# Performance work log

Hardware: AMD Instinct MI355X
Metric: run time of the kernel (lower is better)

## Reference

```python
import jax, jax.numpy as jnp
import numpy as np

B, L, D, H, WIN, EXP = 2, 4096, 1024, 16, 256, 4

def setup_inputs() -> dict:
    key = jax.random.key(0)
    ks = jax.random.split(key, 8)
    F = EXP * D
    p = lambda k, shape: jax.random.normal(k, shape, dtype=jnp.float32) * 0.02
    return {
        "x": jax.random.normal(ks[0], (B, L, D), dtype=jnp.float32),
        "mask": jnp.zeros((B, L), dtype=jnp.float32),  # 0 = local attention everywhere
        "Wq": p(ks[1], (D, D)), "bq": jnp.zeros((D,), jnp.float32),
        "Wk": p(ks[2], (D, D)), "bk": jnp.zeros((D,), jnp.float32),
        "Wv": p(ks[3], (D, D)), "bv": jnp.zeros((D,), jnp.float32),
        "ln_g": jnp.ones((D,), jnp.float32), "ln_b": jnp.zeros((D,), jnp.float32),
        "W1": p(ks[4], (D, F)), "b1": jnp.zeros((F,), jnp.float32),
        "W2": p(ks[5], (F, D)), "b2": jnp.zeros((D,), jnp.float32),
    }


def reference(x, mask, Wq, bq, Wk, bk, Wv, bv, ln_g, ln_b, W1, b1, W2, b2):
    NEG = jnp.asarray(-1e9, x.dtype)
    Bs, Ls, Ds = x.shape
    dh = Ds // H
    c = WIN // 2  # one-sided window size (HF uses attention_window // 2)
    pad = WIN - Ls % WIN
    xp = jnp.pad(x, ((0, 0), (0, pad), (0, 0)))  # pad_token_id == 0
    mp = jnp.pad(mask, ((0, 0), (0, pad)), constant_values=-10000.0)
    S = Ls + pad
    n = S // c  # number of query chunks of size c

    inv_sqrt_dh = jnp.asarray(1.0 / np.sqrt(dh), x.dtype)
    q = ((xp @ Wq + bq) * inv_sqrt_dh).reshape(Bs, S, H, dh)
    k = (xp @ Wk + bk).reshape(Bs, S, H, dh)
    v = (xp @ Wv + bv).reshape(Bs, S, H, dh)

    # pad keys/values by one chunk on each side so query chunk i sees chunks i-1,i,i+1
    kp = jnp.pad(k, ((0, 0), (c, c), (0, 0), (0, 0)))
    vp = jnp.pad(v, ((0, 0), (c, c), (0, 0), (0, 0)))
    kvalid = jnp.pad(mp == 0.0, ((0, 0), (c, c)), constant_values=False)  # [B, S+2c]

    idx = jnp.arange(n)[:, None] * c + jnp.arange(3 * c)[None, :]  # [n, 3c]
    kc = kp[:, idx]   # [B, n, 3c, H, dh]
    vc = vp[:, idx]   # [B, n, 3c, H, dh]
    kvc = kvalid[:, idx]  # [B, n, 3c]
    qc = q.reshape(Bs, n, c, H, dh)

    scores = jnp.einsum('bnphd,bnrhd->bhnpr', qc, kc)  # [B,H,n,c,3c]
    p_ = jnp.arange(c)[:, None]
    r_ = jnp.arange(3 * c)[None, :]
    band = (r_ >= p_) & (r_ <= p_ + 2 * c)  # exact |i-j| <= c band, [c,3c]
    valid = band[None, None, None, :, :] & kvc[:, None, :, None, :]
    scores = jnp.where(valid, scores, NEG)
    probs = jax.nn.softmax(scores, axis=-1)
    attn = jnp.einsum('bhnpr,bnrhd->bnphd', probs, vc).reshape(Bs, S, Ds)

    h = (xp + attn)[:, :Ls]  # residual then drop padding (matches module order)
    mu = jnp.mean(h, axis=-1, keepdims=True)
    var = jnp.var(h, axis=-1, keepdims=True)
    h = (h - mu) / jnp.sqrt(var + 1e-5) * ln_g + ln_b
    out = h + (jax.nn.gelu(h @ W1 + b1, approximate=False) @ W2 + b2)
    return out
```

## Files before the change

kernel.cpp:

```cpp
#include <hip/hip_runtime.h>
#include <hip/hip_bf16.h>
#include <cstdint>

typedef __attribute__((ext_vector_type(8))) short short8;
typedef __attribute__((ext_vector_type(4))) short short4v;
typedef __attribute__((ext_vector_type(4))) float floatx4;

constexpr int B_ = 2, L_ = 4096, D_ = 1024, H_ = 16, DH = 64, F_ = 4096;
constexpr int M_ = B_ * L_;
constexpr int NQKV = 3 * D_;
constexpr int VT_GUARD = 512;

constexpr size_t OFF_XB  = 0;
constexpr size_t OFF_WCT = OFF_XB  + (size_t)M_ * D_ * 2;
constexpr size_t OFF_W1T = OFF_WCT + (size_t)NQKV * D_ * 2;
constexpr size_t OFF_W2T = OFF_W1T + (size_t)F_ * D_ * 2;
constexpr size_t OFF_QKV = OFF_W2T + (size_t)D_ * F_ * 2;
constexpr size_t OFF_VT  = OFF_QKV + (size_t)M_ * NQKV * 2;
constexpr size_t OFF_ATT = OFF_VT  + ((size_t)B_*H_*DH*L_ + 2*VT_GUARD) * 2;
constexpr size_t OFF_HB  = OFF_ATT + (size_t)M_ * D_ * 2;
constexpr size_t OFF_MID = OFF_HB  + (size_t)M_ * D_ * 2;

static __device__ __forceinline__ float b2f(unsigned short u) {
    union { unsigned int i; float f; } v; v.i = ((unsigned int)u) << 16; return v.f;
}

static __device__ __forceinline__ void gload16(const void* g, void* l) {
    __builtin_amdgcn_global_load_lds(
        (const __attribute__((address_space(1))) uint32_t*)g,
        (__attribute__((address_space(3))) uint32_t*)l, 16, 0, 0);
}

__global__ __launch_bounds__(256) void k_cvt_x(const float* __restrict__ x,
                                               __hip_bfloat16* __restrict__ xb) {
    int i = (blockIdx.x * 256 + threadIdx.x) * 8;
    float4 a = *(const float4*)(x + i);
    float4 b = *(const float4*)(x + i + 4);
    alignas(16) __hip_bfloat16 t[8];
    t[0] = __float2bfloat16(a.x); t[1] = __float2bfloat16(a.y);
    t[2] = __float2bfloat16(a.z); t[3] = __float2bfloat16(a.w);
    t[4] = __float2bfloat16(b.x); t[5] = __float2bfloat16(b.y);
    t[6] = __float2bfloat16(b.z); t[7] = __float2bfloat16(b.w);
    *(uint4*)(xb + i) = *(const uint4*)t;
}

__global__ __launch_bounds__(256) void k_tcvt(const float* __restrict__ in,
                                              __hip_bfloat16* __restrict__ out,
                                              int R, int C) {
    __shared__ float t[64][65];
    int tx = threadIdx.x & 63, ty4 = threadIdx.x >> 6;
    int c0 = blockIdx.x * 64, r0 = blockIdx.y * 64;
#pragma unroll
    for (int i = 0; i < 16; i++) {
        int r = ty4 + i * 4;
        t[r][tx] = in[(size_t)(r0 + r) * C + c0 + tx];
    }
    __syncthreads();
#pragma unroll
    for (int i = 0; i < 16; i++) {
        int r = ty4 + i * 4;
        out[(size_t)(c0 + r) * R + r0 + tx] = __float2bfloat16(t[tx][r]);
    }
}

__global__ __launch_bounds__(256) void k_vtrans(const __hip_bfloat16* __restrict__ qkv,
                                                __hip_bfloat16* __restrict__ vtg) {
    __shared__ __hip_bfloat16 t[64][72];
    int tx = threadIdx.x & 63, ty4 = threadIdx.x >> 6;
    int bh = blockIdx.y, b = bh >> 4, h = bh & 15;
    int j0 = blockIdx.x * 64;
#pragma unroll
    for (int i = 0; i < 16; i++) {
        int j = ty4 + i * 4;
        t[j][tx] = qkv[(size_t)(b * L_ + j0 + j) * NQKV + 2 * D_ + h * DH + tx];
    }
    __syncthreads();
#pragma unroll
    for (int i = 0; i < 16; i++) {
        int d = ty4 + i * 4;
        vtg[(long)(bh * DH + d) * L_ + j0 + tx] = t[tx][d];
    }
}

template<int NFRAG, int GM, int EPI, int KTOT, int NBN>
__global__ __launch_bounds__(512, 2)
void k_g8(const __hip_bfloat16* __restrict__ A, const __hip_bfloat16* __restrict__ BT,
          const float* __restrict__ b0p, const float* __restrict__ b1p,
          const float* __restrict__ b2p,
          __hip_bfloat16* __restrict__ obf, float* __restrict__ of32,
          const __hip_bfloat16* __restrict__ hres) {
    constexpr int BN = NFRAG * 64;
    constexpr int KT = KTOT / 64;
    constexpr int PER = GM * NBN;

    __shared__ __hip_bfloat16 AS[2][4 * 4096];
    __shared__ __hip_bfloat16 BS[2][NFRAG * 4096];

    const int tid = threadIdx.x, wave = tid >> 6, lane = tid & 63;
    const int lo = lane & 15, hi = lane >> 4;
    const int wm = wave >> 2, wn = wave & 3;

    const int nwg = gridDim.x, q = nwg >> 3;
    const int bid = blockIdx.x;
    const int swz = (bid & 7) * q + (bid >> 3);
    const int g = swz / PER, r = swz % PER;
    const int bm = g * GM + (r % GM);
    const int bn = r / GM;
    const size_t m0 = (size_t)bm * 256, n0 = (size_t)bn * BN;

    const int srow = tid >> 3;
    const int gcc = (tid & 7) ^ (srow & 7);
    const __hip_bfloat16* aG = A  + (m0 + srow) * (size_t)KTOT + gcc * 8;
    const __hip_bfloat16* bG = BT + (n0 + srow) * (size_t)KTOT + gcc * 8;
    const int ldst = wave * 512;

    int ccr[2];
#pragma unroll
    for (int k = 0; k < 2; ++k) ccr[k] = ((k * 4 + hi) ^ (lo & 7)) * 8;
    const int Ra = wm * 128 + lo;
    const int Rb0 = wn * (NFRAG * 16) + lo;

    floatx4 acc[8][NFRAG] = {};

#define STG_A(buf, sw, tn) gload16(aG + (size_t)(sw) * 64 * KTOT + (size_t)(tn) * 64, \
                                   &AS[buf][(sw) * 4096 + ldst])
#define STG_B(buf, sw, tn) gload16(bG + (size_t)(sw) * 64 * KTOT + (size_t)(tn) * 64, \
                                   &BS[buf][(sw) * 4096 + ldst])

    STG_B(0, 0, 0); STG_B(0, 1, 0);
    if (NFRAG == 4) { STG_B(0, 2, 0); STG_B(0, 3, 0); }
    STG_A(0, 0, 0); STG_A(0, 2, 0); STG_A(0, 1, 0); STG_A(0, 3, 0);
    asm volatile("s_waitcnt vmcnt(0)" ::: "memory");
    __builtin_amdgcn_s_barrier();

    for (int t = 0; t < KT; ++t) {
        const int cur = t & 1, nxt = cur ^ 1;
        const int tn = (t + 1 < KT) ? (t + 1) : 0;
        const __hip_bfloat16* aL = &AS[cur][0];
        const __hip_bfloat16* bL = &BS[cur][0];
        short8 bfr[NFRAG][2], afr[2][2];

#pragma unroll
        for (int gf = 0; gf < NFRAG; ++gf)
#pragma unroll
            for (int k = 0; k < 2; ++k)
                bfr[gf][k] = *(const short8*)(bL + (Rb0 + gf * 16) * 64 + ccr[k]);
#pragma unroll
        for (int f = 0; f < 2; ++f)
#pragma unroll
            for (int k = 0; k < 2; ++k)
                afr[f][k] = *(const short8*)(aL + (Ra + f * 16) * 64 + ccr[k]);
        STG_B(nxt, 0, tn); STG_B(nxt, 1, tn);
        __builtin_amdgcn_s_barrier();
        __builtin_amdgcn_s_setprio(1);
#pragma unroll
        for (int f = 0; f < 2; ++f)
#pragma unroll
            for (int gf = 0; gf < NFRAG; ++gf)
#pragma unroll
                for (int k = 0; k < 2; ++k)
                    acc[f][gf] = __builtin_amdgcn_mfma_f32_16x16x32_bf16(
                        afr[f][k], bfr[gf][k], acc[f][gf], 0, 0, 0);
        __builtin_amdgcn_s_setprio(0);
        __builtin_amdgcn_s_barrier();

#pragma unroll
        for (int f = 0; f < 2; ++f)
#pragma unroll
            for (int k = 0; k < 2; ++k)
                afr[f][k] = *(const short8*)(aL + (Ra + (2 + f) * 16) * 64 + ccr[k]);
        if (NFRAG == 4) { STG_B(nxt, 2, tn); STG_B(nxt, 3, tn); }
        else            { STG_A(nxt, 0, tn); STG_A(nxt, 2, tn); }
        asm volatile("s_waitcnt vmcnt(4)" ::: "memory");
        __builtin_amdgcn_s_barrier();
        __builtin_amdgcn_s_setprio(1);
#pragma unroll
        for (int f = 0; f < 2; ++f)
#pragma unroll
            for (int gf = 0; gf < NFRAG; ++gf)
#pragma unroll
                for (int k = 0; k < 2; ++k)
                    acc[2 + f][gf] = __builtin_amdgcn_mfma_f32_16x16x32_bf16(
                        afr[f][k], bfr[gf][k], acc[2 + f][gf], 0, 0, 0);
        __builtin_amdgcn_s_setprio(0);
        __builtin_amdgcn_s_barrier();

#pragma unroll
        for (int f = 0; f < 2; ++f)
#pragma unroll
            for (int k = 0; k < 2; ++k)
                afr[f][k] = *(const short8*)(aL + (Ra + (4 + f) * 16) * 64 + ccr[k]);
        if (NFRAG == 4) { STG_A(nxt, 0, tn); STG_A(nxt, 2, tn); }
        else            { STG_A(nxt, 1, tn); STG_A(nxt, 3, tn); }
        __builtin_amdgcn_s_barrier();
        __builtin_amdgcn_s_setprio(1);
#pragma unroll
        for (int f = 0; f < 2; ++f)
#pragma unroll
            for (int gf = 0; gf < NFRAG; ++gf)
#pragma unroll
                for (int k = 0; k < 2; ++k)
                    acc[4 + f][gf] = __builtin_amdgcn_mfma_f32_16x16x32_bf16(
                        afr[f][k], bfr[gf][k], acc[4 + f][gf], 0, 0, 0);
        __builtin_amdgcn_s_setprio(0);
        __builtin_amdgcn_s_barrier();

#pragma unroll
        for (int f = 0; f < 2; ++f)
#pragma unroll
            for (int k = 0; k < 2; ++k)
                afr[f][k] = *(const short8*)(aL + (Ra + (6 + f) * 16) * 64 + ccr[k]);
        if (NFRAG == 4) { STG_A(nxt, 1, tn); STG_A(nxt, 3, tn); }
        asm volatile("s_waitcnt vmcnt(2)" ::: "memory");
        __builtin_amdgcn_s_barrier();
        __builtin_amdgcn_s_setprio(1);
#pragma unroll
        for (int f = 0; f < 2; ++f)
#pragma unroll
            for (int gf = 0; gf < NFRAG; ++gf)
#pragma unroll
                for (int k = 0; k < 2; ++k)
                    acc[6 + f][gf] = __builtin_amdgcn_mfma_f32_16x16x32_bf16(
                        afr[f][k], bfr[gf][k], acc[6 + f][gf], 0, 0, 0);
        __builtin_amdgcn_s_setprio(0);
        __builtin_amdgcn_s_barrier();
    }
#undef STG_A
#undef STG_B

#pragma unroll
    for (int mf = 0; mf < 8; ++mf) {
        const int row = (int)m0 + wm * 128 + mf * 16 + hi * 4;
#pragma unroll
        for (int gf = 0; gf < NFRAG; ++gf) {
            const int col = (int)n0 + wn * (NFRAG * 16) + gf * 16 + lo;
#pragma unroll
            for (int rr = 0; rr < 4; ++rr) {
                float v = acc[mf][gf][rr];
                const size_t ro = (size_t)(row + rr);
                if (EPI == 0) {
                    float bia = (col < 1024) ? b0p[col]
                              : (col < 2048 ? b1p[col - 1024] : b2p[col - 2048]);
                    obf[ro * NQKV + col] = __float2bfloat16(v + bia);
                } else if (EPI == 1) {
                    v += b0p[col];
                    v = 0.5f * v * (1.0f + erff(v * 0.70710678118654752440f));
                    obf[ro * F_ + col] = __float2bfloat16(v);
                } else {
                    v += b0p[col];
                    v += b2f(*(const unsigned short*)&hres[ro * D_ + col]);
                    of32[ro * D_ + col] = v;
                }
            }
        }
    }
}

__global__ __launch_bounds__(256, 2)
void k_attn(const __hip_bfloat16* __restrict__ qkv, const float* __restrict__ mask,
            const __hip_bfloat16* __restrict__ vtg, __hip_bfloat16* __restrict__ attnb) {
    constexpr int PS = 296;
    __shared__ __hip_bfloat16 P[4][16 * PS];
    const int tid = threadIdx.x, wave = tid >> 6, lane = tid & 63;
    const int bh = blockIdx.y, b = bh >> 4, h = bh & 15;
    const int q0 = blockIdx.x * 64 + wave * 16;
    const int lo = lane & 15, hi = lane >> 4;

    short8 qf0, qf1;
    {
        const __hip_bfloat16* qb = qkv + (size_t)(b * L_ + q0 + lo) * NQKV + h * DH + hi * 8;
        qf0 = *(const short8*)qb;
        qf1 = *(const short8*)(qb + 32);
    }

    floatx4 sc[17];
    const __hip_bfloat16* kcol = qkv + (size_t)b * L_ * NQKV + D_ + h * DH + hi * 8;
#pragma unroll
    for (int t = 0; t < 17; t++) {
        int jg = q0 - 128 + t * 16 + lo;
        int jc = jg < 0 ? 0 : (jg >= L_ ? L_ - 1 : jg);
        const __hip_bfloat16* kb = kcol + (size_t)jc * NQKV;
        short8 kf0 = *(const short8*)kb;
        short8 kf1 = *(const short8*)(kb + 32);
        floatx4 a = {};
        a = __builtin_amdgcn_mfma_f32_16x16x32_bf16(qf0, kf0, a, 0, 0, 0);
        a = __builtin_amdgcn_mfma_f32_16x16x32_bf16(qf1, kf1, a, 0, 0, 0);
        float mval = mask[b * L_ + jc];
        bool jok = (jg >= 0) && (jg < L_) && (mval == 0.0f);
#pragma unroll
        for (int r = 0; r < 4; r++) {
            int qi = q0 + hi * 4 + r;
            bool ok = jok && (jg >= qi - 128) && (jg <= qi + 128);
            a[r] = ok ? a[r] * 0.125f : -1e9f;
        }
        sc[t] = a;
    }

#pragma unroll
    for (int r = 0; r < 4; r++) {
        float m = -3e38f;
#pragma unroll
        for (int t = 0; t < 17; t++) m = fmaxf(m, sc[t][r]);
        m = fmaxf(m, __shfl_xor(m, 1));
        m = fmaxf(m, __shfl_xor(m, 2));
        m = fmaxf(m, __shfl_xor(m, 4));
        m = fmaxf(m, __shfl_xor(m, 8));
        float s = 0.0f;
#pragma unroll
        for (int t = 0; t < 17; t++) { float e = __expf(sc[t][r] - m); sc[t][r] = e; s += e; }
        s += __shfl_xor(s, 1); s += __shfl_xor(s, 2);
        s += __shfl_xor(s, 4); s += __shfl_xor(s, 8);
        float inv = 1.0f / s;
#pragma unroll
        for (int t = 0; t < 17; t++) sc[t][r] *= inv;
    }

    __hip_bfloat16* Pw = &P[wave][0];
#pragma unroll
    for (int t = 0; t < 17; t++)
#pragma unroll
        for (int r = 0; r < 4; r++)
            Pw[(hi * 4 + r) * PS + t * 16 + lo] = __float2bfloat16(sc[t][r]);
    {
        int zr = lane >> 2, zc = 272 + (lane & 3) * 4;
        __hip_bfloat16 z = __float2bfloat16(0.0f);
#pragma unroll
        for (int i = 0; i < 4; i++) Pw[zr * PS + zc + i] = z;
    }

    floatx4 o[4] = {};
#pragma unroll
    for (int st = 0; st < 9; st++) {
        short8 pa = *(const short8*)(Pw + lo * PS + st * 32 + hi * 8);
        int jb = q0 - 128 + st * 32 + hi * 8;
#pragma unroll
        for (int dt = 0; dt < 4; dt++) {
            const __hip_bfloat16* vb = vtg + (long)(bh * DH + dt * 16 + lo) * L_ + jb;
            short8 vf = *(const short8*)vb;
            o[dt] = __builtin_amdgcn_mfma_f32_16x16x32_bf16(pa, vf, o[dt], 0, 0, 0);
        }
    }

#pragma unroll
    for (int dt = 0; dt < 4; dt++)
#pragma unroll
        for (int r = 0; r < 4; r++) {
            int row = q0 + hi * 4 + r;
            attnb[(size_t)(b * L_ + row) * D_ + h * DH + dt * 16 + lo] =
                __float2bfloat16(o[dt][r]);
        }
}

__global__ __launch_bounds__(256)
void k_ln(const float* __restrict__ x, const __hip_bfloat16* __restrict__ attnb,
          const float* __restrict__ g, const float* __restrict__ bt,
          __hip_bfloat16* __restrict__ hb) {
    const int row = blockIdx.x, tid = threadIdx.x;
    const int c4 = tid * 4;
    float4 xv = *(const float4*)(x + (size_t)row * D_ + c4);
    short4v av = *(const short4v*)(attnb + (size_t)row * D_ + c4);
    float h0 = xv.x + b2f((unsigned short)av[0]);
    float h1 = xv.y + b2f((unsigned short)av[1]);
    float h2 = xv.z + b2f((unsigned short)av[2]);
    float h3 = xv.w + b2f((unsigned short)av[3]);
    float s = h0 + h1 + h2 + h3;
    float q = h0 * h0 + h1 * h1 + h2 * h2 + h3 * h3;
#pragma unroll
    for (int off = 32; off > 0; off >>= 1) {
        s += __shfl_down(s, off);
        q += __shfl_down(q, off);
    }
    __shared__ float red[8];
    int wave = tid >> 6, lane = tid & 63;
    if (lane == 0) { red[wave] = s; red[4 + wave] = q; }
    __syncthreads();
    s = red[0] + red[1] + red[2] + red[3];
    q = red[4] + red[5] + red[6] + red[7];
    float mu = s * (1.0f / D_);
    float var = q * (1.0f / D_) - mu * mu;
    float inv = rsqrtf(var + 1e-5f);
    float4 gv = *(const float4*)(g + c4);
    float4 bv = *(const float4*)(bt + c4);
    alignas(8) __hip_bfloat16 ov[4];
    ov[0] = __float2bfloat16((h0 - mu) * inv * gv.x + bv.x);
    ov[1] = __float2bfloat16((h1 - mu) * inv * gv.y + bv.y);
    ov[2] = __float2bfloat16((h2 - mu) * inv * gv.z + bv.z);
    ov[3] = __float2bfloat16((h3 - mu) * inv * gv.w + bv.w);
    *(short4v*)(hb + (size_t)row * D_ + c4) = *(const short4v*)ov;
}

extern "C" void kernel_launch(void* const* d_in, const int* in_sizes, int n_in,
                              void* d_out, int out_size, void* d_ws, size_t ws_size,
                              hipStream_t stream) {
    const float* x    = (const float*)d_in[0];
    const float* mask = (const float*)d_in[1];
    const float* Wq   = (const float*)d_in[2];
    const float* bq   = (const float*)d_in[3];
    const float* Wk   = (const float*)d_in[4];
    const float* bk   = (const float*)d_in[5];
    const float* Wv   = (const float*)d_in[6];
    const float* bv   = (const float*)d_in[7];
    const float* ln_g = (const float*)d_in[8];
    const float* ln_b = (const float*)d_in[9];
    const float* W1   = (const float*)d_in[10];
    const float* b1   = (const float*)d_in[11];
    const float* W2   = (const float*)d_in[12];
    const float* b2   = (const float*)d_in[13];
    float* out = (float*)d_out;
    char* ws = (char*)d_ws;

    __hip_bfloat16* xb   = (__hip_bfloat16*)(ws + OFF_XB);
    __hip_bfloat16* wct  = (__hip_bfloat16*)(ws + OFF_WCT);
    __hip_bfloat16* w1t  = (__hip_bfloat16*)(ws + OFF_W1T);
    __hip_bfloat16* w2t  = (__hip_bfloat16*)(ws + OFF_W2T);
    __hip_bfloat16* qkvb = (__hip_bfloat16*)(ws + OFF_QKV);
    __hip_bfloat16* vtg  = (__hip_bfloat16*)(ws + OFF_VT) + VT_GUARD;
    __hip_bfloat16* attb = (__hip_bfloat16*)(ws + OFF_ATT);
    __hip_bfloat16* hb   = (__hip_bfloat16*)(ws + OFF_HB);
    __hip_bfloat16* midb = (__hip_bfloat16*)(ws + OFF_MID);

    k_cvt_x<<<(M_ * D_) / 2048, 256, 0, stream>>>(x, xb);
    k_tcvt<<<dim3(D_ / 64, D_ / 64), 256, 0, stream>>>(Wq, wct,                   D_, D_);
    k_tcvt<<<dim3(D_ / 64, D_ / 64), 256, 0, stream>>>(Wk, wct + 1024 * 1024,     D_, D_);
    k_tcvt<<<dim3(D_ / 64, D_ / 64), 256, 0, stream>>>(Wv, wct + 2 * 1024 * 1024, D_, D_);
    k_tcvt<<<dim3(F_ / 64, D_ / 64), 256, 0, stream>>>(W1, w1t, D_, F_);
    k_tcvt<<<dim3(D_ / 64, F_ / 64), 256, 0, stream>>>(W2, w2t, F_, D_);

    k_g8<2, 4, 0, D_, 24><<<768, 512, 0, stream>>>(
        xb, wct, bq, bk, bv, qkvb, nullptr, nullptr);

    k_vtrans<<<dim3(L_ / 64, B_ * H_), 256, 0, stream>>>(qkvb, vtg);
    k_attn<<<dim3(L_ / 64, B_ * H_), 256, 0, stream>>>(qkvb, mask, vtg, attb);

    k_ln<<<M_, 256, 0, stream>>>(x, attb, ln_g, ln_b, hb);

    k_g8<4, 4, 1, D_, 16><<<512, 512, 0, stream>>>(
        hb, w1t, b1, nullptr, nullptr, midb, nullptr, nullptr);
    k_g8<2, 4, 2, F_, 8><<<256, 512, 0, stream>>>(
        midb, w2t, b2, nullptr, nullptr, nullptr, out, hb);
}
```

Before: 505.4 us.

## Issue all next-tile loads upfront and merge GEMM phases by tile width

```diff
diff --git a/kernel.cpp b/kernel.cpp
--- a/kernel.cpp
+++ b/kernel.cpp
@@ -29,6 +29,13 @@
     __builtin_amdgcn_global_load_lds(
         (const __attribute__((address_space(1))) uint32_t*)g,
         (__attribute__((address_space(3))) uint32_t*)l, 16, 0, 0);
+}
+
+template<int N> static __device__ __forceinline__ void waitvm() {
+    if constexpr (N == 2)      asm volatile("s_waitcnt vmcnt(2)" ::: "memory");
+    else if constexpr (N == 6) asm volatile("s_waitcnt vmcnt(6)" ::: "memory");
+    else if constexpr (N == 8) asm volatile("s_waitcnt vmcnt(8)" ::: "memory");
+    else                       asm volatile("s_waitcnt vmcnt(0)" ::: "memory");
 }
 
 __global__ __launch_bounds__(256) void k_cvt_x(const float* __restrict__ x,
@@ -92,6 +99,8 @@
     constexpr int BN = NFRAG * 64;
     constexpr int KT = KTOT / 64;
     constexpr int PER = GM * NBN;
+    constexpr int NPH = (NFRAG == 4) ? 4 : 2;
+    constexpr int MPF = 8 / NPH;
 
     __shared__ __hip_bfloat16 AS[2][4 * 4096];
     __shared__ __hip_bfloat16 BS[2][NFRAG * 4096];
@@ -126,107 +135,65 @@
                                    &AS[buf][(sw) * 4096 + ldst])
 #define STG_B(buf, sw, tn) gload16(bG + (size_t)(sw) * 64 * KTOT + (size_t)(tn) * 64, \
                                    &BS[buf][(sw) * 4096 + ldst])
-
-    STG_B(0, 0, 0); STG_B(0, 1, 0);
-    if (NFRAG == 4) { STG_B(0, 2, 0); STG_B(0, 3, 0); }
-    STG_A(0, 0, 0); STG_A(0, 2, 0); STG_A(0, 1, 0); STG_A(0, 3, 0);
+#define STG_ALL(buf, tn)                                                     \
+    do {                                                                     \
+        STG_B(buf, 0, tn); STG_B(buf, 1, tn);                                \
+        if constexpr (NFRAG == 4) { STG_B(buf, 2, tn); STG_B(buf, 3, tn); }  \
+        STG_A(buf, 0, tn); STG_A(buf, 2, tn);                                \
+        STG_A(buf, 1, tn); STG_A(buf, 3, tn);                                \
+    } while (0)
+
+    STG_ALL(0, 0);
     asm volatile("s_waitcnt vmcnt(0)" ::: "memory");
     __builtin_amdgcn_s_barrier();
 
     for (int t = 0; t < KT; ++t) {
         const int cur = t & 1, nxt = cur ^ 1;
-        const int tn = (t + 1 < KT) ? (t + 1) : 0;
+        const int tn = (t + 1 < KT) ? (t + 1) : t;
         const __hip_bfloat16* aL = &AS[cur][0];
         const __hip_bfloat16* bL = &BS[cur][0];
-        short8 bfr[NFRAG][2], afr[2][2];
-
-#pragma unroll
-        for (int gf = 0; gf < NFRAG; ++gf)
-#pragma unroll
-            for (int k = 0; k < 2; ++k)
-                bfr[gf][k] = *(const short8*)(bL + (Rb0 + gf * 16) * 64 + ccr[k]);
-#pragma unroll
-        for (int f = 0; f < 2; ++f)
-#pragma unroll
-            for (int k = 0; k < 2; ++k)
-                afr[f][k] = *(const short8*)(aL + (Ra + f * 16) * 64 + ccr[k]);
-        STG_B(nxt, 0, tn); STG_B(nxt, 1, tn);
-        __builtin_amdgcn_s_barrier();
-        __builtin_amdgcn_s_setprio(1);
-#pragma unroll
-        for (int f = 0; f < 2; ++f)
-#pragma unroll
-            for (int gf = 0; gf < NFRAG; ++gf)
+        short8 bfr[NFRAG][2];
+
+#pragma unroll
+        for (int p = 0; p < NPH; ++p) {
+            short8 afr[MPF][2];
+            if (p == 0) {
+#pragma unroll
+                for (int gf = 0; gf < NFRAG; ++gf)
+#pragma unroll
+                    for (int k = 0; k < 2; ++k)
+                        bfr[gf][k] = *(const short8*)(bL + (Rb0 + gf * 16) * 64 + ccr[k]);
+            }
+#pragma unroll
+            for (int f = 0; f < MPF; ++f)
 #pragma unroll
                 for (int k = 0; k < 2; ++k)
-                    acc[f][gf] = __builtin_amdgcn_mfma_f32_16x16x32_bf16(
-                        afr[f][k], bfr[gf][k], acc[f][gf], 0, 0, 0);
-        __builtin_amdgcn_s_setprio(0);
-        __builtin_amdgcn_s_barrier();
-
-#pragma unroll
-        for (int f = 0; f < 2; ++f)
-#pragma unroll
-            for (int k = 0; k < 2; ++k)
-                afr[f][k] = *(const short8*)(aL + (Ra + (2 + f) * 16) * 64 + ccr[k]);
-        if (NFRAG == 4) { STG_B(nxt, 2, tn); STG_B(nxt, 3, tn); }
-        else            { STG_A(nxt, 0, tn); STG_A(nxt, 2, tn); }
-        asm volatile("s_waitcnt vmcnt(4)" ::: "memory");
-        __builtin_amdgcn_s_barrier();
-        __builtin_amdgcn_s_setprio(1);
-#pragma unroll
-        for (int f = 0; f < 2; ++f)
-#pragma unroll
-            for (int gf = 0; gf < NFRAG; ++gf)
-#pragma unroll
-                for (int k = 0; k < 2; ++k)
-                    acc[2 + f][gf] = __builtin_amdgcn_mfma_f32_16x16x32_bf16(
-                        afr[f][k], bfr[gf][k], acc[2 + f][gf], 0, 0, 0);
-        __builtin_amdgcn_s_setprio(0);
-        __builtin_amdgcn_s_barrier();
-
-#pragma unroll
-        for (int f = 0; f < 2; ++f)
-#pragma unroll
-            for (int k = 0; k < 2; ++k)
-                afr[f][k] = *(const short8*)(aL + (Ra + (4 + f) * 16) * 64 + ccr[k]);
-        if (NFRAG == 4) { STG_A(nxt, 0, tn); STG_A(nxt, 2, tn); }
-        else            { STG_A(nxt, 1, tn); STG_A(nxt, 3, tn); }
-        __builtin_amdgcn_s_barrier();
-        __builtin_amdgcn_s_setprio(1);
-#pragma unroll
-        for (int f = 0; f < 2; ++f)
-#pragma unroll
-            for (int gf = 0; gf < NFRAG; ++gf)
-#pragma unroll
-                for (int k = 0; k < 2; ++k)
-                    acc[4 + f][gf] = __builtin_amdgcn_mfma_f32_16x16x32_bf16(
-                        afr[f][k], bfr[gf][k], acc[4 + f][gf], 0, 0, 0);
-        __builtin_amdgcn_s_setprio(0);
-        __builtin_amdgcn_s_barrier();
-
-#pragma unroll
-        for (int f = 0; f < 2; ++f)
-#pragma unroll
-            for (int k = 0; k < 2; ++k)
-                afr[f][k] = *(const short8*)(aL + (Ra + (6 + f) * 16) * 64 + ccr[k]);
-        if (NFRAG == 4) { STG_A(nxt, 1, tn); STG_A(nxt, 3, tn); }
-        asm volatile("s_waitcnt vmcnt(2)" ::: "memory");
-        __builtin_amdgcn_s_barrier();
-        __builtin_amdgcn_s_setprio(1);
-#pragma unroll
-        for (int f = 0; f < 2; ++f)
-#pragma unroll
-            for (int gf = 0; gf < NFRAG; ++gf)
-#pragma unroll
-                for (int k = 0; k < 2; ++k)
-                    acc[6 + f][gf] = __builtin_amdgcn_mfma_f32_16x16x32_bf16(
-                        afr[f][k], bfr[gf][k], acc[6 + f][gf], 0, 0, 0);
-        __builtin_amdgcn_s_setprio(0);
-        __builtin_amdgcn_s_barrier();
+                    afr[f][k] = *(const short8*)(aL + (Ra + (p * MPF + f) * 16) * 64 + ccr[k]);
+            if (p == 0) STG_ALL(nxt, tn);
+            __builtin_amdgcn_s_barrier();
+            __builtin_amdgcn_s_setprio(1);
+#pragma unroll
+            for (int f = 0; f < MPF; ++f)
+#pragma unroll
+                for (int gf = 0; gf < NFRAG; ++gf)
+#pragma unroll
+                    for (int k = 0; k < 2; ++k)
+                        acc[p * MPF + f][gf] = __builtin_amdgcn_mfma_f32_16x16x32_bf16(
+                            afr[f][k], bfr[gf][k], acc[p * MPF + f][gf], 0, 0, 0);
+            __builtin_amdgcn_s_setprio(0);
+            if constexpr (NPH == 4) {
+                if (p == 1) waitvm<8>();
+                if (p == 3) waitvm<2>();
+            } else {
+                if (p == 0) waitvm<6>();
+                if (p == 1) waitvm<2>();
+            }
+            __builtin_amdgcn_s_barrier();
+        }
     }
 #undef STG_A
 #undef STG_B
+#undef STG_ALL
 
 #pragma unroll
     for (int mf = 0; mf < 8; ++mf) {
@@ -436,6 +403,6 @@
 
     k_g8<4, 4, 1, D_, 16><<<512, 512, 0, stream>>>(
         hb, w1t, b1, nullptr, nullptr, midb, nullptr, nullptr);
-    k_g8<2, 4, 2, F_, 8><<<256, 512, 0, stream>>>(
+    k_g8<2, 1, 2, F_, 8><<<256, 512, 0, stream>>>(
         midb, w2t, b2, nullptr, nullptr, nullptr, out, hb);
 }
```

Result: no change. 500.9 us (-0.9%).
